# Kernel optimization log

Measured on AMD Instinct MI355X. Metric: run time of the kernel, lower is better.

Reference implementation:

```python
import jax, jax.numpy as jnp
import numpy as np

B, S, D = 8, 1024, 1024
H, DH = 16, 64  # num_attention_heads, attention_head_size; H*DH == D


def setup_inputs() -> dict:
    key = jax.random.key(0)
    ks = jax.random.split(key, 6)
    scale = 0.02
    return {
        "hidden_states": jax.random.normal(ks[0], (B, S, D), jnp.float32),
        "right_hidden_states": jax.random.normal(ks[1], (B, S, D), jnp.float32),
        "attention_mask": jnp.ones((B, S, S), jnp.float32),
        "Wq": jax.random.normal(ks[2], (D, H * DH), jnp.float32) * scale,
        "bq": jnp.zeros((H * DH,), jnp.float32),
        "Wk": jax.random.normal(ks[3], (D, H * DH), jnp.float32) * scale,
        "bk": jnp.zeros((H * DH,), jnp.float32),
        "Wv": jax.random.normal(ks[4], (D, H * DH), jnp.float32) * scale,
        "bv": jnp.zeros((H * DH,), jnp.float32),
    }


def _split_heads(x, b):
    # (B, S, H*DH) -> (B, H, S, DH)
    return x.reshape(b, -1, H, DH).transpose(0, 2, 1, 3)


def reference(hidden_states, right_hidden_states, attention_mask, Wq, bq, Wk, bk, Wv, bv):
    b = hidden_states.shape[0]
    q = _split_heads(hidden_states @ Wq + bq, b)          # (B,H,Sq,DH)
    k = _split_heads(right_hidden_states @ Wk + bk, b)    # (B,H,Sk,DH)
    v = _split_heads(right_hidden_states @ Wv + bv, b)    # (B,H,Sk,DH)

    scores = jnp.einsum("bhqd,bhkd->bhqk", q, k) / jnp.sqrt(jnp.asarray(DH, q.dtype))
    scores = jnp.sum(scores, axis=1, keepdims=True)       # (B,1,Sq,Sk) head-summed

    ext = (1.0 - attention_mask[:, None, :, :].astype(scores.dtype)) * -1e9
    probs = jax.nn.softmax(scores + ext, axis=-1)         # (B,1,Sq,Sk)

    ctx = jnp.matmul(probs, v)                            # broadcast -> (B,H,Sq,DH)
    # Faithful to original: reshape WITHOUT transposing heads back.
    return ctx.reshape(b, -1, H * DH)                     # (B,Sq,H*DH)
```

## Files before the change

kernel.cpp:

```cpp
#include <hip/hip_runtime.h>
#include <stdint.h>

constexpr int S = 1024;
constexpr int D = 1024;
constexpr int NB = 8;

typedef __bf16 bf16x8 __attribute__((ext_vector_type(8)));
typedef float floatx4 __attribute__((ext_vector_type(4)));

#define AS1 __attribute__((address_space(1)))
#define AS3 __attribute__((address_space(3)))

__device__ __forceinline__ unsigned short f2bf(float f) {
  unsigned u = __builtin_bit_cast(unsigned, f);
  u += 0x7fffu + ((u >> 16) & 1u);
  return (unsigned short)(u >> 16);
}

__device__ __forceinline__ void gload16(const void* g, void* l) {
  __builtin_amdgcn_global_load_lds((const AS1 unsigned int*)g, (AS3 unsigned int*)l, 16, 0, 0);
}

__global__ __launch_bounds__(256) void cast2_bf16_kernel(const float4* __restrict__ a,
                                                         const float4* __restrict__ b,
                                                         ushort4* __restrict__ oa,
                                                         ushort4* __restrict__ ob, int n4) {
  int i = blockIdx.x * 256 + threadIdx.x;
  const float4* src;
  ushort4* dst;
  int j;
  if (i < n4) {
    src = a; dst = oa; j = i;
  } else {
    src = b; dst = ob; j = i - n4;
  }
  float4 v = src[j];
  ushort4 o;
  o.x = f2bf(v.x); o.y = f2bf(v.y); o.z = f2bf(v.z); o.w = f2bf(v.w);
  dst[j] = o;
}

__global__ __launch_bounds__(256) void transpose_w3_kernel(const float* __restrict__ Wq,
                                                           const float* __restrict__ Wk,
                                                           const float* __restrict__ Wv,
                                                           unsigned short* __restrict__ Wcat) {
  __shared__ float tile[32][33];
  const float* W = (blockIdx.z == 0) ? Wq : (blockIdx.z == 1) ? Wk : Wv;
  unsigned short* Wt = Wcat + (long long)blockIdx.z * D * D;
  int bx = blockIdx.x * 32;
  int by = blockIdx.y * 32;
  int x = threadIdx.x & 31;
  int y0 = threadIdx.x >> 5;
  for (int i = 0; i < 4; ++i) {
    int y = y0 + i * 8;
    tile[y][x] = W[(by + y) * D + bx + x];
  }
  __syncthreads();
  for (int i = 0; i < 4; ++i) {
    int y = y0 + i * 8;
    Wt[(long long)(bx + y) * D + by + x] = f2bf(tile[x][y]);
  }
}

__global__ __launch_bounds__(256) void gemm_qkv_kernel(
    const unsigned short* __restrict__ hsb, const unsigned short* __restrict__ rhsb,
    const unsigned short* __restrict__ Wcat, unsigned short* __restrict__ Qm,
    unsigned short* __restrict__ Km, unsigned short* __restrict__ Vmt,
    const float* __restrict__ bq, const float* __restrict__ bk, const float* __restrict__ bv) {
  __shared__ __align__(16) unsigned short As[128 * 32];
  __shared__ __align__(16) unsigned short Bs[128 * 32];
  const int tid = threadIdx.x;
  const int lane = tid & 63;
  const int w = tid >> 6;
  const long long n0g = (long long)blockIdx.x * 128;
  const int seg = (int)(n0g >> 10);
  const long long m0 = (long long)blockIdx.y * 128;
  const unsigned short* A = (seg == 0) ? hsb : rhsb;
  const unsigned short* Bt = Wcat + n0g * D;
  const float* bias = (seg == 0) ? bq : (seg == 1) ? bk : bv;

  const int idx0 = tid, idx1 = tid + 256;
  const unsigned short* aG0 = A + (m0 + (idx0 >> 2)) * D + (idx0 & 3) * 8;
  const unsigned short* aG1 = A + (m0 + (idx1 >> 2)) * D + (idx1 & 3) * 8;
  const unsigned short* bG0 = Bt + (long long)(idx0 >> 2) * D + (idx0 & 3) * 8;
  const unsigned short* bG1 = Bt + (long long)(idx1 >> 2) * D + (idx1 & 3) * 8;
  unsigned short* aL0 = As + w * 512;
  unsigned short* aL1 = As + w * 512 + 2048;
  unsigned short* bL0 = Bs + w * 512;
  unsigned short* bL1 = Bs + w * 512 + 2048;

  floatx4 zero4 = {0.f, 0.f, 0.f, 0.f};
  floatx4 acc[4][4];
  for (int i = 0; i < 4; ++i)
    for (int j = 0; j < 4; ++j) acc[i][j] = zero4;

  const int r15 = lane & 15;
  const int quad = lane >> 4;
  const int wm = (w >> 1) * 64;
  const int wn = (w & 1) * 64;

  for (int k0 = 0; k0 < D; k0 += 32) {
    gload16(aG0 + k0, aL0);
    gload16(aG1 + k0, aL1);
    gload16(bG0 + k0, bL0);
    gload16(bG1 + k0, bL1);
    __syncthreads();
    bf16x8 af[4], bfr[4];
    for (int t = 0; t < 4; ++t) {
      af[t] = *reinterpret_cast<const bf16x8*>(As + (wm + t * 16 + r15) * 32 + quad * 8);
      bfr[t] = *reinterpret_cast<const bf16x8*>(Bs + (wn + t * 16 + r15) * 32 + quad * 8);
    }
    for (int mt = 0; mt < 4; ++mt)
      for (int nt = 0; nt < 4; ++nt)
        acc[mt][nt] =
            __builtin_amdgcn_mfma_f32_16x16x32_bf16(af[mt], bfr[nt], acc[mt][nt], 0, 0, 0);
    __syncthreads();
  }

  const long long nloc0 = n0g & 1023;
  for (int mt = 0; mt < 4; ++mt) {
    for (int nt = 0; nt < 4; ++nt) {
      const long long mrow = m0 + wm + mt * 16 + quad * 4;
      const long long nc = nloc0 + wn + nt * 16 + r15;
      const float bval = bias[nc];
      floatx4 v = acc[mt][nt];
      for (int e = 0; e < 4; ++e) {
        float val = v[e] + bval;
        long long m = mrow + e;
        if (seg == 0) {
          Qm[m * D + nc] = f2bf(val);
        } else if (seg == 1) {
          Km[m * D + nc] = f2bf(val);
        } else {
          Vmt[(m >> 10) * (long long)(S * D) + nc * S + (m & 1023)] = f2bf(val);
        }
      }
    }
  }
}

template <int MODE>
__global__ __launch_bounds__(256) void gemm_nt_kernel(
    const unsigned short* __restrict__ A, int lda, long long strideA,
    const unsigned short* __restrict__ Bt, int ldb, long long strideB, float* __restrict__ C,
    long long strideC, float alpha, int K) {
  __shared__ __align__(16) unsigned short As[128 * 32];
  __shared__ __align__(16) unsigned short Bs[128 * 32];
  const int tid = threadIdx.x;
  const int lane = tid & 63;
  const int w = tid >> 6;
  const int z = blockIdx.z;
  const long long m0 = (long long)blockIdx.y * 128;
  const long long n0 = (long long)blockIdx.x * 128;
  A += (long long)z * strideA;
  Bt += (long long)z * strideB;

  const int idx0 = tid, idx1 = tid + 256;
  const unsigned short* aG0 = A + (m0 + (idx0 >> 2)) * lda + (idx0 & 3) * 8;
  const unsigned short* aG1 = A + (m0 + (idx1 >> 2)) * lda + (idx1 & 3) * 8;
  const unsigned short* bG0 = Bt + (n0 + (idx0 >> 2)) * ldb + (idx0 & 3) * 8;
  const unsigned short* bG1 = Bt + (n0 + (idx1 >> 2)) * ldb + (idx1 & 3) * 8;
  unsigned short* aL0 = As + w * 512;
  unsigned short* aL1 = As + w * 512 + 2048;
  unsigned short* bL0 = Bs + w * 512;
  unsigned short* bL1 = Bs + w * 512 + 2048;

  floatx4 zero4 = {0.f, 0.f, 0.f, 0.f};
  floatx4 acc[4][4];
  for (int i = 0; i < 4; ++i)
    for (int j = 0; j < 4; ++j) acc[i][j] = zero4;

  const int r15 = lane & 15;
  const int quad = lane >> 4;
  const int wm = (w >> 1) * 64;
  const int wn = (w & 1) * 64;

  for (int k0 = 0; k0 < K; k0 += 32) {
    gload16(aG0 + k0, aL0);
    gload16(aG1 + k0, aL1);
    gload16(bG0 + k0, bL0);
    gload16(bG1 + k0, bL1);
    __syncthreads();
    bf16x8 af[4], bfr[4];
    for (int t = 0; t < 4; ++t) {
      af[t] = *reinterpret_cast<const bf16x8*>(As + (wm + t * 16 + r15) * 32 + quad * 8);
      bfr[t] = *reinterpret_cast<const bf16x8*>(Bs + (wn + t * 16 + r15) * 32 + quad * 8);
    }
    for (int mt = 0; mt < 4; ++mt)
      for (int nt = 0; nt < 4; ++nt)
        acc[mt][nt] =
            __builtin_amdgcn_mfma_f32_16x16x32_bf16(af[mt], bfr[nt], acc[mt][nt], 0, 0, 0);
    __syncthreads();
  }

  for (int mt = 0; mt < 4; ++mt) {
    for (int nt = 0; nt < 4; ++nt) {
      const long long mrow = m0 + wm + mt * 16 + quad * 4;
      const long long ncol = n0 + wn + nt * 16 + r15;
      floatx4 v = acc[mt][nt];
      for (int e = 0; e < 4; ++e) {
        float val = v[e] * alpha;
        long long m = mrow + e;
        if constexpr (MODE == 2) {
          C[(long long)z * strideC + m * S + ncol] = val;
        } else {
          C[(long long)z * strideC + (ncol >> 6) * (long long)(S * 64) + m * 64 + (ncol & 63)] =
              val;
        }
      }
    }
  }
}

__global__ __launch_bounds__(256) void softmax_kernel(const float* scores,
                                                      const float* __restrict__ mask,
                                                      unsigned short* probs) {
  const long long row = blockIdx.x;
  const float4* s4 = (const float4*)(scores + row * S);
  const float4* m4 = (const float4*)(mask + row * S);
  ushort4* p4 = (ushort4*)(probs + row * 2048);
  const int tid = threadIdx.x;
  const int lane = tid & 63, w = tid >> 6;
  float4 sv = s4[tid];
  float4 mv = m4[tid];
  float v[4] = {sv.x + (1.0f - mv.x) * -1e9f, sv.y + (1.0f - mv.y) * -1e9f,
                sv.z + (1.0f - mv.z) * -1e9f, sv.w + (1.0f - mv.w) * -1e9f};
  float mx = fmaxf(fmaxf(v[0], v[1]), fmaxf(v[2], v[3]));
  for (int off = 32; off; off >>= 1) mx = fmaxf(mx, __shfl_xor(mx, off, 64));
  __shared__ float redm[4], reds[4];
  if (lane == 0) redm[w] = mx;
  __syncthreads();
  mx = fmaxf(fmaxf(redm[0], redm[1]), fmaxf(redm[2], redm[3]));
  float sum = 0.f;
  for (int i = 0; i < 4; ++i) {
    v[i] = __expf(v[i] - mx);
    sum += v[i];
  }
  for (int off = 32; off; off >>= 1) sum += __shfl_xor(sum, off, 64);
  if (lane == 0) reds[w] = sum;
  __syncthreads();
  sum = reds[0] + reds[1] + reds[2] + reds[3];
  float inv = 1.0f / sum;
  ushort4 o;
  o.x = f2bf(v[0] * inv);
  o.y = f2bf(v[1] * inv);
  o.z = f2bf(v[2] * inv);
  o.w = f2bf(v[3] * inv);
  p4[tid] = o;
}

extern "C" void kernel_launch(void* const* d_in, const int* in_sizes, int n_in, void* d_out,
                              int out_size, void* d_ws, size_t ws_size, hipStream_t stream) {
  const float* hs = (const float*)d_in[0];
  const float* rhs = (const float*)d_in[1];
  const float* mask = (const float*)d_in[2];
  const float* Wq = (const float*)d_in[3];
  const float* bq = (const float*)d_in[4];
  const float* Wk = (const float*)d_in[5];
  const float* bk = (const float*)d_in[6];
  const float* Wv = (const float*)d_in[7];
  const float* bv = (const float*)d_in[8];
  float* out = (float*)d_out;
  char* ws = (char*)d_ws;
  const size_t MB = 1ull << 20;
  unsigned short* Wcat = (unsigned short*)(ws + 0 * MB);
  unsigned short* hsb = (unsigned short*)(ws + 6 * MB);
  unsigned short* rhsb = (unsigned short*)(ws + 22 * MB);
  unsigned short* Qm = (unsigned short*)(ws + 38 * MB);
  unsigned short* Km = (unsigned short*)(ws + 54 * MB);
  unsigned short* Vmt = (unsigned short*)(ws + 70 * MB);
  float* scores = (float*)(ws + 6 * MB);
  unsigned short* probs = (unsigned short*)scores;

  const int n4 = NB * S * D / 4;
  cast2_bf16_kernel<<<2 * n4 / 256, 256, 0, stream>>>((const float4*)hs, (const float4*)rhs,
                                                      (ushort4*)hsb, (ushort4*)rhsb, n4);
  transpose_w3_kernel<<<dim3(32, 32, 3), 256, 0, stream>>>(Wq, Wk, Wv, Wcat);

  gemm_qkv_kernel<<<dim3(24, 64), 256, 0, stream>>>(hsb, rhsb, Wcat, Qm, Km, Vmt, bq, bk, bv);

  gemm_nt_kernel<2><<<dim3(8, 8, NB), 256, 0, stream>>>(Qm, D, (long long)S * D, Km, D,
                                                        (long long)S * D, scores,
                                                        (long long)S * S, 0.125f, D);
  softmax_kernel<<<NB * S, 256, 0, stream>>>(scores, mask, probs);
  gemm_nt_kernel<3><<<dim3(8, 8, NB), 256, 0, stream>>>(probs, 2048, (long long)S * 2048, Vmt, D,
                                                        (long long)S * D, out, (long long)S * D,
                                                        1.f, D);
}
```

Measured before the change: 316.5 us.

## Use K=64 swizzled LDS tiles, XCD-aware block mapping, and fuse prep kernels

The GEMM kernels now stage 64-wide K slices into LDS with an XOR swizzle, which halves the number of barrier pairs and avoids LDS bank conflicts on fragment reads. Blocks are remapped from 3D grids to a flat index so that tiles sharing operands, or the same batch, land on the same XCD for better L2 reuse. The softmax rows are remapped the same way. The bf16 cast and weight-transpose kernels are merged into one launch to save a launch. LDS use per block doubles, which may lower occupancy.

```diff
diff --git a/kernel.cpp b/kernel.cpp
--- a/kernel.cpp
+++ b/kernel.cpp
@@ -21,73 +21,82 @@
   __builtin_amdgcn_global_load_lds((const AS1 unsigned int*)g, (AS3 unsigned int*)l, 16, 0, 0);
 }
 
-__global__ __launch_bounds__(256) void cast2_bf16_kernel(const float4* __restrict__ a,
-                                                         const float4* __restrict__ b,
-                                                         ushort4* __restrict__ oa,
-                                                         ushort4* __restrict__ ob, int n4) {
-  int i = blockIdx.x * 256 + threadIdx.x;
-  const float4* src;
-  ushort4* dst;
-  int j;
-  if (i < n4) {
-    src = a; dst = oa; j = i;
+__global__ __launch_bounds__(256) void prep_kernel(const float4* __restrict__ hs4,
+                                                   const float4* __restrict__ rhs4,
+                                                   ushort4* __restrict__ hsb4,
+                                                   ushort4* __restrict__ rhsb4, int n4,
+                                                   const float* __restrict__ Wq,
+                                                   const float* __restrict__ Wk,
+                                                   const float* __restrict__ Wv,
+                                                   unsigned short* __restrict__ Wcat) {
+  __shared__ float tile[32][33];
+  const int bid = blockIdx.x;
+  if (bid < 16384) {
+    int i = bid * 256 + threadIdx.x;
+    const float4* src;
+    ushort4* dst;
+    int j;
+    if (i < n4) {
+      src = hs4; dst = hsb4; j = i;
+    } else {
+      src = rhs4; dst = rhsb4; j = i - n4;
+    }
+    float4 v = src[j];
+    ushort4 o;
+    o.x = f2bf(v.x); o.y = f2bf(v.y); o.z = f2bf(v.z); o.w = f2bf(v.w);
+    dst[j] = o;
   } else {
-    src = b; dst = ob; j = i - n4;
-  }
-  float4 v = src[j];
-  ushort4 o;
-  o.x = f2bf(v.x); o.y = f2bf(v.y); o.z = f2bf(v.z); o.w = f2bf(v.w);
-  dst[j] = o;
-}
-
-__global__ __launch_bounds__(256) void transpose_w3_kernel(const float* __restrict__ Wq,
-                                                           const float* __restrict__ Wk,
-                                                           const float* __restrict__ Wv,
-                                                           unsigned short* __restrict__ Wcat) {
-  __shared__ float tile[32][33];
-  const float* W = (blockIdx.z == 0) ? Wq : (blockIdx.z == 1) ? Wk : Wv;
-  unsigned short* Wt = Wcat + (long long)blockIdx.z * D * D;
-  int bx = blockIdx.x * 32;
-  int by = blockIdx.y * 32;
-  int x = threadIdx.x & 31;
-  int y0 = threadIdx.x >> 5;
-  for (int i = 0; i < 4; ++i) {
-    int y = y0 + i * 8;
-    tile[y][x] = W[(by + y) * D + bx + x];
-  }
-  __syncthreads();
-  for (int i = 0; i < 4; ++i) {
-    int y = y0 + i * 8;
-    Wt[(long long)(bx + y) * D + by + x] = f2bf(tile[x][y]);
-  }
-}
+    const int t = bid - 16384;
+    const int z = t >> 10;
+    const int r = t & 1023;
+    const float* W = (z == 0) ? Wq : (z == 1) ? Wk : Wv;
+    unsigned short* Wt = Wcat + (long long)z * D * D;
+    const int bx = (r & 31) * 32;
+    const int by = (r >> 5) * 32;
+    const int x = threadIdx.x & 31;
+    const int y0 = threadIdx.x >> 5;
+    for (int i = 0; i < 4; ++i) {
+      int y = y0 + i * 8;
+      tile[y][x] = W[(by + y) * D + bx + x];
+    }
+    __syncthreads();
+    for (int i = 0; i < 4; ++i) {
+      int y = y0 + i * 8;
+      Wt[(long long)(bx + y) * D + by + x] = f2bf(tile[x][y]);
+    }
+  }
+}
+
 
 __global__ __launch_bounds__(256) void gemm_qkv_kernel(
     const unsigned short* __restrict__ hsb, const unsigned short* __restrict__ rhsb,
     const unsigned short* __restrict__ Wcat, unsigned short* __restrict__ Qm,
     unsigned short* __restrict__ Km, unsigned short* __restrict__ Vmt,
     const float* __restrict__ bq, const float* __restrict__ bk, const float* __restrict__ bv) {
-  __shared__ __align__(16) unsigned short As[128 * 32];
-  __shared__ __align__(16) unsigned short Bs[128 * 32];
+  __shared__ __align__(16) unsigned short As[128 * 64];
+  __shared__ __align__(16) unsigned short Bs[128 * 64];
   const int tid = threadIdx.x;
   const int lane = tid & 63;
   const int w = tid >> 6;
-  const long long n0g = (long long)blockIdx.x * 128;
-  const int seg = (int)(n0g >> 10);
-  const long long m0 = (long long)blockIdx.y * 128;
+  const int bid = blockIdx.x;
+  const int local = bid >> 3;
+  const int n_tile = (bid & 7) * 3 + (local % 3);
+  const long long m0 = (long long)(local / 3) * 128;
+  const long long n0g = (long long)n_tile * 128;
+  const int seg = n_tile >> 3;
   const unsigned short* A = (seg == 0) ? hsb : rhsb;
   const unsigned short* Bt = Wcat + n0g * D;
   const float* bias = (seg == 0) ? bq : (seg == 1) ? bk : bv;
 
-  const int idx0 = tid, idx1 = tid + 256;
-  const unsigned short* aG0 = A + (m0 + (idx0 >> 2)) * D + (idx0 & 3) * 8;
-  const unsigned short* aG1 = A + (m0 + (idx1 >> 2)) * D + (idx1 & 3) * 8;
-  const unsigned short* bG0 = Bt + (long long)(idx0 >> 2) * D + (idx0 & 3) * 8;
-  const unsigned short* bG1 = Bt + (long long)(idx1 >> 2) * D + (idx1 & 3) * 8;
-  unsigned short* aL0 = As + w * 512;
-  unsigned short* aL1 = As + w * 512 + 2048;
-  unsigned short* bL0 = Bs + w * 512;
-  unsigned short* bL1 = Bs + w * 512 + 2048;
+  const unsigned short* aG[4];
+  const unsigned short* bG[4];
+  for (int j = 0; j < 4; ++j) {
+    int idx = tid + j * 256;
+    int row = idx >> 3;
+    int cg = (idx & 7) ^ (row & 7);
+    aG[j] = A + (m0 + row) * D + cg * 8;
+    bG[j] = Bt + (long long)row * D + cg * 8;
+  }
 
   floatx4 zero4 = {0.f, 0.f, 0.f, 0.f};
   floatx4 acc[4][4];
@@ -99,21 +108,22 @@
   const int wm = (w >> 1) * 64;
   const int wn = (w & 1) * 64;
 
-  for (int k0 = 0; k0 < D; k0 += 32) {
-    gload16(aG0 + k0, aL0);
-    gload16(aG1 + k0, aL1);
-    gload16(bG0 + k0, bL0);
-    gload16(bG1 + k0, bL1);
-    __syncthreads();
-    bf16x8 af[4], bfr[4];
-    for (int t = 0; t < 4; ++t) {
-      af[t] = *reinterpret_cast<const bf16x8*>(As + (wm + t * 16 + r15) * 32 + quad * 8);
-      bfr[t] = *reinterpret_cast<const bf16x8*>(Bs + (wn + t * 16 + r15) * 32 + quad * 8);
-    }
-    for (int mt = 0; mt < 4; ++mt)
-      for (int nt = 0; nt < 4; ++nt)
-        acc[mt][nt] =
-            __builtin_amdgcn_mfma_f32_16x16x32_bf16(af[mt], bfr[nt], acc[mt][nt], 0, 0, 0);
+  for (int k0 = 0; k0 < D; k0 += 64) {
+    for (int j = 0; j < 4; ++j) gload16(aG[j] + k0, As + j * 2048 + w * 512);
+    for (int j = 0; j < 4; ++j) gload16(bG[j] + k0, Bs + j * 2048 + w * 512);
+    __syncthreads();
+    for (int kk = 0; kk < 2; ++kk) {
+      const int ca = ((kk << 2) | quad) ^ (r15 & 7);
+      bf16x8 af[4], bfr[4];
+      for (int t = 0; t < 4; ++t) {
+        af[t] = *reinterpret_cast<const bf16x8*>(As + (wm + t * 16 + r15) * 64 + ca * 8);
+        bfr[t] = *reinterpret_cast<const bf16x8*>(Bs + (wn + t * 16 + r15) * 64 + ca * 8);
+      }
+      for (int mt = 0; mt < 4; ++mt)
+        for (int nt = 0; nt < 4; ++nt)
+          acc[mt][nt] =
+              __builtin_amdgcn_mfma_f32_16x16x32_bf16(af[mt], bfr[nt], acc[mt][nt], 0, 0, 0);
+    }
     __syncthreads();
   }
 
@@ -144,26 +154,28 @@
     const unsigned short* __restrict__ A, int lda, long long strideA,
     const unsigned short* __restrict__ Bt, int ldb, long long strideB, float* __restrict__ C,
     long long strideC, float alpha, int K) {
-  __shared__ __align__(16) unsigned short As[128 * 32];
-  __shared__ __align__(16) unsigned short Bs[128 * 32];
+  __shared__ __align__(16) unsigned short As[128 * 64];
+  __shared__ __align__(16) unsigned short Bs[128 * 64];
   const int tid = threadIdx.x;
   const int lane = tid & 63;
   const int w = tid >> 6;
-  const int z = blockIdx.z;
-  const long long m0 = (long long)blockIdx.y * 128;
-  const long long n0 = (long long)blockIdx.x * 128;
+  const int bid = blockIdx.x;
+  const int z = bid & 7;
+  const int local = bid >> 3;
+  const long long m0 = (long long)(local & 7) * 128;
+  const long long n0 = (long long)(local >> 3) * 128;
   A += (long long)z * strideA;
   Bt += (long long)z * strideB;
 
-  const int idx0 = tid, idx1 = tid + 256;
-  const unsigned short* aG0 = A + (m0 + (idx0 >> 2)) * lda + (idx0 & 3) * 8;
-  const unsigned short* aG1 = A + (m0 + (idx1 >> 2)) * lda + (idx1 & 3) * 8;
-  const unsigned short* bG0 = Bt + (n0 + (idx0 >> 2)) * ldb + (idx0 & 3) * 8;
-  const unsigned short* bG1 = Bt + (n0 + (idx1 >> 2)) * ldb + (idx1 & 3) * 8;
-  unsigned short* aL0 = As + w * 512;
-  unsigned short* aL1 = As + w * 512 + 2048;
-  unsigned short* bL0 = Bs + w * 512;
-  unsigned short* bL1 = Bs + w * 512 + 2048;
+  const unsigned short* aG[4];
+  const unsigned short* bG[4];
+  for (int j = 0; j < 4; ++j) {
+    int idx = tid + j * 256;
+    int row = idx >> 3;
+    int cg = (idx & 7) ^ (row & 7);
+    aG[j] = A + (m0 + row) * lda + cg * 8;
+    bG[j] = Bt + (n0 + row) * ldb + cg * 8;
+  }
 
   floatx4 zero4 = {0.f, 0.f, 0.f, 0.f};
   floatx4 acc[4][4];
@@ -175,21 +187,22 @@
   const int wm = (w >> 1) * 64;
   const int wn = (w & 1) * 64;
 
-  for (int k0 = 0; k0 < K; k0 += 32) {
-    gload16(aG0 + k0, aL0);
-    gload16(aG1 + k0, aL1);
-    gload16(bG0 + k0, bL0);
-    gload16(bG1 + k0, bL1);
-    __syncthreads();
-    bf16x8 af[4], bfr[4];
-    for (int t = 0; t < 4; ++t) {
-      af[t] = *reinterpret_cast<const bf16x8*>(As + (wm + t * 16 + r15) * 32 + quad * 8);
-      bfr[t] = *reinterpret_cast<const bf16x8*>(Bs + (wn + t * 16 + r15) * 32 + quad * 8);
-    }
-    for (int mt = 0; mt < 4; ++mt)
-      for (int nt = 0; nt < 4; ++nt)
-        acc[mt][nt] =
-            __builtin_amdgcn_mfma_f32_16x16x32_bf16(af[mt], bfr[nt], acc[mt][nt], 0, 0, 0);
+  for (int k0 = 0; k0 < K; k0 += 64) {
+    for (int j = 0; j < 4; ++j) gload16(aG[j] + k0, As + j * 2048 + w * 512);
+    for (int j = 0; j < 4; ++j) gload16(bG[j] + k0, Bs + j * 2048 + w * 512);
+    __syncthreads();
+    for (int kk = 0; kk < 2; ++kk) {
+      const int ca = ((kk << 2) | quad) ^ (r15 & 7);
+      bf16x8 af[4], bfr[4];
+      for (int t = 0; t < 4; ++t) {
+        af[t] = *reinterpret_cast<const bf16x8*>(As + (wm + t * 16 + r15) * 64 + ca * 8);
+        bfr[t] = *reinterpret_cast<const bf16x8*>(Bs + (wn + t * 16 + r15) * 64 + ca * 8);
+      }
+      for (int mt = 0; mt < 4; ++mt)
+        for (int nt = 0; nt < 4; ++nt)
+          acc[mt][nt] =
+              __builtin_amdgcn_mfma_f32_16x16x32_bf16(af[mt], bfr[nt], acc[mt][nt], 0, 0, 0);
+    }
     __syncthreads();
   }
 
@@ -215,7 +228,8 @@
 __global__ __launch_bounds__(256) void softmax_kernel(const float* scores,
                                                       const float* __restrict__ mask,
                                                       unsigned short* probs) {
-  const long long row = blockIdx.x;
+  const int bid = blockIdx.x;
+  const long long row = (long long)(bid & 7) * 1024 + (bid >> 3);
   const float4* s4 = (const float4*)(scores + row * S);
   const float4* m4 = (const float4*)(mask + row * S);
   ushort4* p4 = (ushort4*)(probs + row * 2048);
@@ -273,17 +287,15 @@
   unsigned short* probs = (unsigned short*)scores;
 
   const int n4 = NB * S * D / 4;
-  cast2_bf16_kernel<<<2 * n4 / 256, 256, 0, stream>>>((const float4*)hs, (const float4*)rhs,
-                                                      (ushort4*)hsb, (ushort4*)rhsb, n4);
-  transpose_w3_kernel<<<dim3(32, 32, 3), 256, 0, stream>>>(Wq, Wk, Wv, Wcat);
-
-  gemm_qkv_kernel<<<dim3(24, 64), 256, 0, stream>>>(hsb, rhsb, Wcat, Qm, Km, Vmt, bq, bk, bv);
-
-  gemm_nt_kernel<2><<<dim3(8, 8, NB), 256, 0, stream>>>(Qm, D, (long long)S * D, Km, D,
-                                                        (long long)S * D, scores,
-                                                        (long long)S * S, 0.125f, D);
+  prep_kernel<<<16384 + 3072, 256, 0, stream>>>((const float4*)hs, (const float4*)rhs,
+                                                (ushort4*)hsb, (ushort4*)rhsb, n4, Wq, Wk, Wv,
+                                                Wcat);
+
+  gemm_qkv_kernel<<<1536, 256, 0, stream>>>(hsb, rhsb, Wcat, Qm, Km, Vmt, bq, bk, bv);
+
+  gemm_nt_kernel<2><<<512, 256, 0, stream>>>(Qm, D, (long long)S * D, Km, D, (long long)S * D,
+                                             scores, (long long)S * S, 0.125f, D);
   softmax_kernel<<<NB * S, 256, 0, stream>>>(scores, mask, probs);
-  gemm_nt_kernel<3><<<dim3(8, 8, NB), 256, 0, stream>>>(probs, 2048, (long long)S * 2048, Vmt, D,
-                                                        (long long)S * D, out, (long long)S * D,
-                                                        1.f, D);
-}
+  gemm_nt_kernel<3><<<512, 256, 0, stream>>>(probs, 2048, (long long)S * 2048, Vmt, D,
+                                             (long long)S * D, out, (long long)S * D, 1.f, D);
+}
```

After: 304.2 us. -3.9%, faster.
